# Optimization experiments

Measured on AMD Instinct MI355X. Metric: run time of the kernel, lower is better.

Reference implementation:

```python
import jax, jax.numpy as jnp
import numpy as np

B, C, S, H, Wd = 512, 32, 8, 6, 6   # batch, in_channels, size_primary_caps, in_h, in_w
O, OW = 10, 16                      # out_height, out_width
IN_CAPS = C * H * Wd                # 1152
ITER = 3                            # routing iterations


def setup_inputs() -> dict:
    key = jax.random.key(0)
    k1, k2 = jax.random.split(key)
    x = jax.random.normal(k1, (B, C, S, H, Wd), dtype=jnp.float32)
    stdv = 1.0 / np.sqrt(S)
    W = jax.random.uniform(k2, (1, O, IN_CAPS, OW, S), dtype=jnp.float32,
                           minval=-stdv, maxval=stdv)
    return {"x": x, "W": W}


def squash(s, axis=-1):
    n2 = jnp.sum(s * s, axis=axis, keepdims=True)
    return (n2 / (1.0 + n2)) * s / jnp.sqrt(n2)


def reference(x, W):
    bsz = x.shape[0]
    # torch: x.reshape(b,1,-1,S,1); row-major reshape is identical in jnp
    xr = x.reshape(bsz, IN_CAPS, S)             # [B, in_caps, S]
    # W @ x : [1,O,I,OW,S] @ [B,1,I,S,1] -> [B,O,I,OW]
    u = jnp.einsum('oiws,bis->boiw', W[0], xr)  # [B, O, in_caps, OW]
    b = jnp.zeros((bsz, O, IN_CAPS, 1), dtype=u.dtype)
    v = None
    for _ in range(ITER):
        c = jax.nn.softmax(b, axis=1)           # softmax over out_height (dim=-3)
        s = jnp.sum(u * c, axis=2)              # [B, O, OW]
        v = squash(s, axis=-1)                  # [B, O, OW]
        agreement = jnp.einsum('boiw,bow->boi', u, v)[..., None]
        b = b + agreement
    return v
```

## Files before the change

kernel.cpp:

```cpp
#include <hip/hip_runtime.h>
#include <cstddef>
#include <cstdint>


typedef _Float16 h2 __attribute__((ext_vector_type(2)));

constexpr int O_ = 10, I_ = 1152, W_ = 16, S_ = 8;
constexpr int BQ = 2;
constexpr int NTH = 1024, NWV = 16;
constexpr int SLOTS = NWV * 4;
constexpr int KSEQ = I_ / SLOTS;
constexpr int WROW = O_ * W_ * S_;

union U32H2 { uint32_t u; h2 h; };
__device__ __forceinline__ h2 as_h2(uint32_t u) { U32H2 c; c.u = u; return c.h; }
__device__ __forceinline__ uint32_t as_u32(h2 h) { U32H2 c; c.h = h; return c.u; }

__device__ __forceinline__ float dpp_sum16(float v) {
  int t;
  t = __builtin_amdgcn_update_dpp(0, __float_as_int(v), 0xB1, 0xF, 0xF, true);
  v += __int_as_float(t);
  t = __builtin_amdgcn_update_dpp(0, __float_as_int(v), 0x4E, 0xF, 0xF, true);
  v += __int_as_float(t);
  t = __builtin_amdgcn_update_dpp(0, __float_as_int(v), 0x141, 0xF, 0xF, true);
  v += __int_as_float(t);
  t = __builtin_amdgcn_update_dpp(0, __float_as_int(v), 0x140, 0xF, 0xF, true);
  v += __int_as_float(t);
  return v;
}

constexpr int W4TOT = O_ * I_ * W_ * S_ / 4;
__global__ __launch_bounds__(256) void wprep(const float4* __restrict__ Wg,
                                             uint2* __restrict__ Wt) {
  int idx = blockIdx.x * 256 + threadIdx.x;
  if (idx >= W4TOT) return;
  int w2 = idx & 31;
  int oi = idx >> 5;
  int o = oi / I_;
  int i = oi - o * I_;
  float4 v = Wg[idx];
  h2 p0 = {(_Float16)v.x, (_Float16)v.y};
  h2 p1 = {(_Float16)v.z, (_Float16)v.w};
  uint2 pk;
  pk.x = as_u32(p0);
  pk.y = as_u32(p1);
  Wt[(i * O_ + o) * 32 + w2] = pk;
}

__global__ __launch_bounds__(NTH, 1) void digitcaps_fused(
    const float* __restrict__ xg, const _Float16* __restrict__ Wt,
    float* __restrict__ out) {
  __shared__ _Float16 xl[BQ * I_ * S_];
  __shared__ float s_buf[NWV][BQ][O_][W_];
  __shared__ float vcur[BQ][O_ * W_];
  __shared__ float v1s[BQ][O_ * W_];

  const int tid = threadIdx.x, blk = blockIdx.x;
  const int wave = tid >> 6, lane = tid & 63;
  const int wg = lane & 15;
  const int isub = lane >> 4;

  {
    const float4* xb = (const float4*)(xg + (size_t)blk * (BQ * I_ * S_));
    uint2* xw = (uint2*)xl;
#pragma unroll
    for (int j = 0; j < 5; ++j) {
      int f = j * NTH + tid;
      if (f < BQ * I_ * S_ / 4) {
        float4 v = xb[f];
        h2 p0 = {(_Float16)v.x, (_Float16)v.y};
        h2 p1 = {(_Float16)v.z, (_Float16)v.w};
        uint2 pk;
        pk.x = as_u32(p0);
        pk.y = as_u32(p1);
        xw[f] = pk;
      }
    }
  }
  __syncthreads();

  const int ib = wave * 4 + isub;

  for (int pass = 0; pass < 3; ++pass) {
    float S[BQ][O_];
#pragma unroll
    for (int b = 0; b < BQ; ++b)
#pragma unroll
      for (int o = 0; o < O_; ++o) S[b][o] = 0.f;

    if (pass == 0) {
#pragma unroll 2
      for (int k = 0; k < KSEQ; ++k) {
        const int i = ib + SLOTS * k;
        uint32_t xr[BQ][4];
#pragma unroll
        for (int b = 0; b < BQ; ++b) {
          uint4 t = *(const uint4*)&xl[(b * I_ + i) * S_];
          xr[b][0] = t.x; xr[b][1] = t.y; xr[b][2] = t.z; xr[b][3] = t.w;
        }
        const _Float16* wi = Wt + (size_t)i * WROW + wg * S_;
#pragma unroll
        for (int o = 0; o < O_; ++o) {
          uint4 wv = *(const uint4*)(wi + o * (W_ * S_));
#pragma unroll
          for (int b = 0; b < BQ; ++b) {
            float u = __builtin_amdgcn_fdot2(as_h2(wv.x), as_h2(xr[b][0]),
                       __builtin_amdgcn_fdot2(as_h2(wv.y), as_h2(xr[b][1]),
                        __builtin_amdgcn_fdot2(as_h2(wv.z), as_h2(xr[b][2]),
                         __builtin_amdgcn_fdot2(as_h2(wv.w), as_h2(xr[b][3]),
                                                0.f, false), false), false), false);
            S[b][o] += u;
          }
        }
      }
    } else {
      float vr[BQ][O_];
#pragma unroll
      for (int b = 0; b < BQ; ++b)
#pragma unroll
        for (int o = 0; o < O_; ++o) vr[b][o] = vcur[b][o * W_ + wg];

#pragma unroll 2
      for (int k = 0; k < KSEQ; ++k) {
        const int i = ib + SLOTS * k;
        uint32_t xr[BQ][4];
#pragma unroll
        for (int b = 0; b < BQ; ++b) {
          uint4 t = *(const uint4*)&xl[(b * I_ + i) * S_];
          xr[b][0] = t.x; xr[b][1] = t.y; xr[b][2] = t.z; xr[b][3] = t.w;
        }
        const _Float16* wi = Wt + (size_t)i * WROW + wg * S_;
        float U[BQ][O_];
        float bl[BQ][O_];
#pragma unroll
        for (int o = 0; o < O_; ++o) {
          uint4 wv = *(const uint4*)(wi + o * (W_ * S_));
#pragma unroll
          for (int b = 0; b < BQ; ++b) {
            float u = __builtin_amdgcn_fdot2(as_h2(wv.x), as_h2(xr[b][0]),
                       __builtin_amdgcn_fdot2(as_h2(wv.y), as_h2(xr[b][1]),
                        __builtin_amdgcn_fdot2(as_h2(wv.z), as_h2(xr[b][2]),
                         __builtin_amdgcn_fdot2(as_h2(wv.w), as_h2(xr[b][3]),
                                                0.f, false), false), false), false);
            U[b][o] = u;
            bl[b][o] = dpp_sum16(u * vr[b][o]);
          }
        }
#pragma unroll
        for (int b = 0; b < BQ; ++b) {
          float m = bl[b][0];
#pragma unroll
          for (int o = 1; o < O_; ++o) m = fmaxf(m, bl[b][o]);
          float es = 0.f;
#pragma unroll
          for (int o = 0; o < O_; ++o) { bl[b][o] = __expf(bl[b][o] - m); es += bl[b][o]; }
          const float inv = 1.0f / es;
#pragma unroll
          for (int o = 0; o < O_; ++o) S[b][o] += (bl[b][o] * inv) * U[b][o];
        }
      }
    }

#pragma unroll
    for (int b = 0; b < BQ; ++b)
#pragma unroll
      for (int o = 0; o < O_; ++o) {
        float s = S[b][o];
        s += __shfl_xor(s, 16);
        s += __shfl_xor(s, 32);
        S[b][o] = s;
      }
    if (isub == 0) {
#pragma unroll
      for (int b = 0; b < BQ; ++b)
#pragma unroll
        for (int o = 0; o < O_; ++o) s_buf[wave][b][o][wg] = S[b][o];
    }
    __syncthreads();

    if (tid < BQ * O_ * W_) {
      const int bb = tid / (O_ * W_);
      const int r = tid % (O_ * W_);
      float s = 0.f;
#pragma unroll
      for (int wv = 0; wv < NWV; ++wv) s += s_buf[wv][bb][r >> 4][r & 15];
      if (pass == 0) s *= 0.1f;
      float n2 = s * s;
      n2 += __shfl_xor(n2, 1);
      n2 += __shfl_xor(n2, 2);
      n2 += __shfl_xor(n2, 4);
      n2 += __shfl_xor(n2, 8);
      const float v = s * sqrtf(n2) / (1.0f + n2);
      if (pass == 0)      { vcur[bb][r] = v; v1s[bb][r] = v; }
      else if (pass == 1) { vcur[bb][r] = v1s[bb][r] + v; }
      else                { out[((size_t)(blk * BQ) + bb) * (O_ * W_) + r] = v; }
    }
    __syncthreads();
  }
}

extern "C" void kernel_launch(void* const* d_in, const int* in_sizes, int n_in,
                              void* d_out, int out_size, void* d_ws, size_t ws_size,
                              hipStream_t stream) {
  const float* x = (const float*)d_in[0];
  const float* W = (const float*)d_in[1];
  float* out = (float*)d_out;
  _Float16* Wt = (_Float16*)d_ws;

  hipLaunchKernelGGL(wprep, dim3((W4TOT + 255) / 256), dim3(256), 0, stream,
                     (const float4*)W, (uint2*)Wt);
  hipLaunchKernelGGL(digitcaps_fused, dim3(512 / BQ), dim3(NTH), 0, stream,
                     x, Wt, out);
}
```

Before: 156.1 us.

## Pack two batches into half2 for routing passes and drop softmax max-subtraction

Splits the first pass from the routing passes. In the routing passes it packs the two batch items' u and v values into fp16 pairs, so the agreement products, the xor-shuffle reductions and the weighted sum accumulation run as packed half operations. It also drops the max-subtraction before the exponentials and swaps the scalar conversions for cvt_pkrtz. This cuts VALU work in the softmax-heavy passes, at the cost of accumulating S in fp16 across 18 iterations and four shuffles, which risks precision loss and overflow in exp without the max shift.

```diff
diff --git a/kernel.cpp b/kernel.cpp
--- a/kernel.cpp
+++ b/kernel.cpp
@@ -4,6 +4,7 @@
 
 
 typedef _Float16 h2 __attribute__((ext_vector_type(2)));
+typedef __fp16 fp16v2 __attribute__((ext_vector_type(2)));
 
 constexpr int O_ = 10, I_ = 1152, W_ = 16, S_ = 8;
 constexpr int BQ = 2;
@@ -12,21 +13,11 @@
 constexpr int KSEQ = I_ / SLOTS;
 constexpr int WROW = O_ * W_ * S_;
 
-union U32H2 { uint32_t u; h2 h; };
+union U32H2 { uint32_t u; h2 h; fp16v2 f; };
 __device__ __forceinline__ h2 as_h2(uint32_t u) { U32H2 c; c.u = u; return c.h; }
 __device__ __forceinline__ uint32_t as_u32(h2 h) { U32H2 c; c.h = h; return c.u; }
-
-__device__ __forceinline__ float dpp_sum16(float v) {
-  int t;
-  t = __builtin_amdgcn_update_dpp(0, __float_as_int(v), 0xB1, 0xF, 0xF, true);
-  v += __int_as_float(t);
-  t = __builtin_amdgcn_update_dpp(0, __float_as_int(v), 0x4E, 0xF, 0xF, true);
-  v += __int_as_float(t);
-  t = __builtin_amdgcn_update_dpp(0, __float_as_int(v), 0x141, 0xF, 0xF, true);
-  v += __int_as_float(t);
-  t = __builtin_amdgcn_update_dpp(0, __float_as_int(v), 0x140, 0xF, 0xF, true);
-  v += __int_as_float(t);
-  return v;
+__device__ __forceinline__ h2 cvt_pk(float a, float b) {
+  U32H2 c; c.f = __builtin_amdgcn_cvt_pkrtz(a, b); return c.h;
 }
 
 constexpr int W4TOT = O_ * I_ * W_ * S_ / 4;
@@ -39,12 +30,18 @@
   int o = oi / I_;
   int i = oi - o * I_;
   float4 v = Wg[idx];
-  h2 p0 = {(_Float16)v.x, (_Float16)v.y};
-  h2 p1 = {(_Float16)v.z, (_Float16)v.w};
   uint2 pk;
-  pk.x = as_u32(p0);
-  pk.y = as_u32(p1);
+  pk.x = as_u32(cvt_pk(v.x, v.y));
+  pk.y = as_u32(cvt_pk(v.z, v.w));
   Wt[(i * O_ + o) * 32 + w2] = pk;
+}
+
+__device__ __forceinline__ float dot8(const uint4& wv, const uint32_t* xr) {
+  return __builtin_amdgcn_fdot2(as_h2(wv.x), as_h2(xr[0]),
+          __builtin_amdgcn_fdot2(as_h2(wv.y), as_h2(xr[1]),
+           __builtin_amdgcn_fdot2(as_h2(wv.z), as_h2(xr[2]),
+            __builtin_amdgcn_fdot2(as_h2(wv.w), as_h2(xr[3]),
+                                   0.f, false), false), false), false);
 }
 
 __global__ __launch_bounds__(NTH, 1) void digitcaps_fused(
@@ -68,11 +65,9 @@
       int f = j * NTH + tid;
       if (f < BQ * I_ * S_ / 4) {
         float4 v = xb[f];
-        h2 p0 = {(_Float16)v.x, (_Float16)v.y};
-        h2 p1 = {(_Float16)v.z, (_Float16)v.w};
         uint2 pk;
-        pk.x = as_u32(p0);
-        pk.y = as_u32(p1);
+        pk.x = as_u32(cvt_pk(v.x, v.y));
+        pk.y = as_u32(cvt_pk(v.z, v.w));
         xw[f] = pk;
       }
     }
@@ -81,86 +76,30 @@
 
   const int ib = wave * 4 + isub;
 
-  for (int pass = 0; pass < 3; ++pass) {
+  {
     float S[BQ][O_];
 #pragma unroll
     for (int b = 0; b < BQ; ++b)
 #pragma unroll
       for (int o = 0; o < O_; ++o) S[b][o] = 0.f;
 
-    if (pass == 0) {
 #pragma unroll 2
-      for (int k = 0; k < KSEQ; ++k) {
-        const int i = ib + SLOTS * k;
-        uint32_t xr[BQ][4];
-#pragma unroll
-        for (int b = 0; b < BQ; ++b) {
-          uint4 t = *(const uint4*)&xl[(b * I_ + i) * S_];
-          xr[b][0] = t.x; xr[b][1] = t.y; xr[b][2] = t.z; xr[b][3] = t.w;
-        }
-        const _Float16* wi = Wt + (size_t)i * WROW + wg * S_;
-#pragma unroll
-        for (int o = 0; o < O_; ++o) {
-          uint4 wv = *(const uint4*)(wi + o * (W_ * S_));
-#pragma unroll
-          for (int b = 0; b < BQ; ++b) {
-            float u = __builtin_amdgcn_fdot2(as_h2(wv.x), as_h2(xr[b][0]),
-                       __builtin_amdgcn_fdot2(as_h2(wv.y), as_h2(xr[b][1]),
-                        __builtin_amdgcn_fdot2(as_h2(wv.z), as_h2(xr[b][2]),
-                         __builtin_amdgcn_fdot2(as_h2(wv.w), as_h2(xr[b][3]),
-                                                0.f, false), false), false), false);
-            S[b][o] += u;
-          }
-        }
-      }
-    } else {
-      float vr[BQ][O_];
-#pragma unroll
-      for (int b = 0; b < BQ; ++b)
-#pragma unroll
-        for (int o = 0; o < O_; ++o) vr[b][o] = vcur[b][o * W_ + wg];
-
-#pragma unroll 2
-      for (int k = 0; k < KSEQ; ++k) {
-        const int i = ib + SLOTS * k;
-        uint32_t xr[BQ][4];
-#pragma unroll
-        for (int b = 0; b < BQ; ++b) {
-          uint4 t = *(const uint4*)&xl[(b * I_ + i) * S_];
-          xr[b][0] = t.x; xr[b][1] = t.y; xr[b][2] = t.z; xr[b][3] = t.w;
-        }
-        const _Float16* wi = Wt + (size_t)i * WROW + wg * S_;
-        float U[BQ][O_];
-        float bl[BQ][O_];
-#pragma unroll
-        for (int o = 0; o < O_; ++o) {
-          uint4 wv = *(const uint4*)(wi + o * (W_ * S_));
-#pragma unroll
-          for (int b = 0; b < BQ; ++b) {
-            float u = __builtin_amdgcn_fdot2(as_h2(wv.x), as_h2(xr[b][0]),
-                       __builtin_amdgcn_fdot2(as_h2(wv.y), as_h2(xr[b][1]),
-                        __builtin_amdgcn_fdot2(as_h2(wv.z), as_h2(xr[b][2]),
-                         __builtin_amdgcn_fdot2(as_h2(wv.w), as_h2(xr[b][3]),
-                                                0.f, false), false), false), false);
-            U[b][o] = u;
-            bl[b][o] = dpp_sum16(u * vr[b][o]);
-          }
-        }
-#pragma unroll
-        for (int b = 0; b < BQ; ++b) {
-          float m = bl[b][0];
-#pragma unroll
-          for (int o = 1; o < O_; ++o) m = fmaxf(m, bl[b][o]);
-          float es = 0.f;
-#pragma unroll
-          for (int o = 0; o < O_; ++o) { bl[b][o] = __expf(bl[b][o] - m); es += bl[b][o]; }
-          const float inv = 1.0f / es;
-#pragma unroll
-          for (int o = 0; o < O_; ++o) S[b][o] += (bl[b][o] * inv) * U[b][o];
-        }
-      }
-    }
-
+    for (int k = 0; k < KSEQ; ++k) {
+      const int i = ib + SLOTS * k;
+      uint32_t xr[BQ][4];
+#pragma unroll
+      for (int b = 0; b < BQ; ++b) {
+        uint4 t = *(const uint4*)&xl[(b * I_ + i) * S_];
+        xr[b][0] = t.x; xr[b][1] = t.y; xr[b][2] = t.z; xr[b][3] = t.w;
+      }
+      const _Float16* wi = Wt + (size_t)i * WROW + wg * S_;
+#pragma unroll
+      for (int o = 0; o < O_; ++o) {
+        uint4 wv = *(const uint4*)(wi + o * (W_ * S_));
+#pragma unroll
+        for (int b = 0; b < BQ; ++b) S[b][o] += dot8(wv, xr[b]);
+      }
+    }
 #pragma unroll
     for (int b = 0; b < BQ; ++b)
 #pragma unroll
@@ -184,16 +123,96 @@
       float s = 0.f;
 #pragma unroll
       for (int wv = 0; wv < NWV; ++wv) s += s_buf[wv][bb][r >> 4][r & 15];
-      if (pass == 0) s *= 0.1f;
+      s *= 0.1f;
       float n2 = s * s;
       n2 += __shfl_xor(n2, 1);
       n2 += __shfl_xor(n2, 2);
       n2 += __shfl_xor(n2, 4);
       n2 += __shfl_xor(n2, 8);
       const float v = s * sqrtf(n2) / (1.0f + n2);
-      if (pass == 0)      { vcur[bb][r] = v; v1s[bb][r] = v; }
-      else if (pass == 1) { vcur[bb][r] = v1s[bb][r] + v; }
-      else                { out[((size_t)(blk * BQ) + bb) * (O_ * W_) + r] = v; }
+      vcur[bb][r] = v;
+      v1s[bb][r] = v;
+    }
+    __syncthreads();
+  }
+
+  for (int pass = 1; pass < 3; ++pass) {
+    h2 vrpk[O_];
+#pragma unroll
+    for (int o = 0; o < O_; ++o)
+      vrpk[o] = cvt_pk(vcur[0][o * W_ + wg], vcur[1][o * W_ + wg]);
+    h2 Spk[O_];
+#pragma unroll
+    for (int o = 0; o < O_; ++o) Spk[o] = h2{(_Float16)0, (_Float16)0};
+
+#pragma unroll 2
+    for (int k = 0; k < KSEQ; ++k) {
+      const int i = ib + SLOTS * k;
+      uint32_t xr[BQ][4];
+#pragma unroll
+      for (int b = 0; b < BQ; ++b) {
+        uint4 t = *(const uint4*)&xl[(b * I_ + i) * S_];
+        xr[b][0] = t.x; xr[b][1] = t.y; xr[b][2] = t.z; xr[b][3] = t.w;
+      }
+      const _Float16* wi = Wt + (size_t)i * WROW + wg * S_;
+      h2 upk[O_], ppk[O_];
+#pragma unroll
+      for (int o = 0; o < O_; ++o) {
+        uint4 wv = *(const uint4*)(wi + o * (W_ * S_));
+        float u0 = dot8(wv, xr[0]);
+        float u1 = dot8(wv, xr[1]);
+        upk[o] = cvt_pk(u0, u1);
+        ppk[o] = upk[o] * vrpk[o];
+      }
+#pragma unroll
+      for (int o = 0; o < O_; ++o) {
+#pragma unroll
+        for (int d = 1; d <= 8; d <<= 1)
+          ppk[o] = ppk[o] + as_h2((uint32_t)__shfl_xor((int)as_u32(ppk[o]), d));
+      }
+      float e0[O_], e1[O_];
+      float es0 = 0.f, es1 = 0.f;
+#pragma unroll
+      for (int o = 0; o < O_; ++o) {
+        e0[o] = __expf((float)ppk[o][0]); es0 += e0[o];
+        e1[o] = __expf((float)ppk[o][1]); es1 += e1[o];
+      }
+      const float inv0 = 1.0f / es0, inv1 = 1.0f / es1;
+#pragma unroll
+      for (int o = 0; o < O_; ++o) {
+        h2 c = cvt_pk(e0[o] * inv0, e1[o] * inv1);
+        Spk[o] = Spk[o] + c * upk[o];
+      }
+    }
+
+#pragma unroll
+    for (int o = 0; o < O_; ++o) {
+      Spk[o] = Spk[o] + as_h2((uint32_t)__shfl_xor((int)as_u32(Spk[o]), 16));
+      Spk[o] = Spk[o] + as_h2((uint32_t)__shfl_xor((int)as_u32(Spk[o]), 32));
+    }
+    if (isub == 0) {
+#pragma unroll
+      for (int o = 0; o < O_; ++o) {
+        s_buf[wave][0][o][wg] = (float)Spk[o][0];
+        s_buf[wave][1][o][wg] = (float)Spk[o][1];
+      }
+    }
+    __syncthreads();
+
+    if (tid < BQ * O_ * W_) {
+      const int bb = tid / (O_ * W_);
+      const int r = tid % (O_ * W_);
+      float s = 0.f;
+#pragma unroll
+      for (int wv = 0; wv < NWV; ++wv) s += s_buf[wv][bb][r >> 4][r & 15];
+      float n2 = s * s;
+      n2 += __shfl_xor(n2, 1);
+      n2 += __shfl_xor(n2, 2);
+      n2 += __shfl_xor(n2, 4);
+      n2 += __shfl_xor(n2, 8);
+      const float v = s * sqrtf(n2) / (1.0f + n2);
+      if (pass == 1)  vcur[bb][r] = v1s[bb][r] + v;
+      else            out[((size_t)(blk * BQ) + bb) * (O_ * W_) + r] = v;
     }
     __syncthreads();
   }
```

Measured after the change: 156.6 us. About the same (+0.4%).
